# Optimization experiments

Hardware: AMD Instinct MI355X
Metric: run time of the kernel (lower is better)

## Reference

```python
import jax, jax.numpy as jnp
import numpy as np

T, B, D, H = 512, 64, 512, 512


def setup_inputs() -> dict:
    key = jax.random.key(0)
    k_x, k_wi, k_wh = jax.random.split(key, 3)
    x = jax.random.normal(k_x, (T, B, D), dtype=jnp.float32)
    h0 = jnp.zeros((B, H), dtype=jnp.float32)
    # orthogonal(sqrt(2))-like scale approximated with scaled normal weights
    Wi = jax.random.normal(k_wi, (D, 3 * H), dtype=jnp.float32) * (1.0 / np.sqrt(D))
    Wh = jax.random.normal(k_wh, (H, 3 * H), dtype=jnp.float32) * (1.0 / np.sqrt(H))
    bi = jnp.zeros((3 * H,), dtype=jnp.float32)
    bhn = jnp.zeros((H,), dtype=jnp.float32)
    return {"x": x, "h0": h0, "Wi": Wi, "Wh": Wh, "bi": bi, "bhn": bhn}


def reference(x, h0, Wi, Wh, bi, bhn):
    # Flax GRUCell scanned over time. Gate order: (r, z, n).
    # Input path has bias bi; hidden path is bias-free except candidate (bhn).
    def step(h, xt):
        gi = xt @ Wi + bi              # [B, 3H]
        gh = h @ Wh                    # [B, 3H]
        i_r, i_z, i_n = jnp.split(gi, 3, axis=-1)
        h_r, h_z, h_n = jnp.split(gh, 3, axis=-1)
        r = jax.nn.sigmoid(i_r + h_r)
        z = jax.nn.sigmoid(i_z + h_z)
        n = jnp.tanh(i_n + r * (h_n + bhn))
        h_new = (1.0 - z) * n + z * h  # [B, H]
        return h_new, h_new            # y == new hidden state in GRUCell

    _, ys = jax.lax.scan(step, h0, x)  # ys: [T, B, H]; final carry == ys[-1]
    return ys
```

## Files before the change

### kernel.cpp

```cpp
#include <hip/hip_runtime.h>


#define T_STEPS 512
#define NWORK 32
#define CWG 8
#define NCL 4
#define NB_LAUNCH 256
#define FSTRIDE 16

typedef __attribute__((ext_vector_type(8))) short bhalf8;
typedef __attribute__((ext_vector_type(4))) float floatx4;

__device__ inline float bf2f(unsigned short u) {
  union { unsigned u; float f; } v; v.u = ((unsigned)u) << 16; return v.f;
}
__device__ inline unsigned short f2bf(float f) {
  union { float f; unsigned u; } v; v.f = f;
  unsigned x = v.u;
  return (unsigned short)((x + 0x7fffu + ((x >> 16) & 1u)) >> 16);
}

__device__ inline void gload_lds16(const void* g, void* l) {
  __builtin_amdgcn_global_load_lds(
      (const __attribute__((address_space(1))) void*)g,
      (__attribute__((address_space(3))) void*)l, 16, 0, 0);
}

#define O_BAR 0
#define O_HB  4096
#define O_WIT 69632
#define O_WHT 1642496
#define O_GI  3215360
#define O_XB  103878656ULL
#define WS_NEED 137433088ULL

__device__ inline unsigned short* HS(char* ws, int t) {
  return (t == 0) ? (unsigned short*)(ws + O_HB)
                  : (unsigned short*)(ws + O_XB + (long)(t - 1) * 65536);
}

__global__ void prep_kernel(const float* __restrict__ x, const float* __restrict__ h0,
                            const float* __restrict__ Wi, const float* __restrict__ Wh,
                            char* __restrict__ ws) {
  unsigned short* Xb  = (unsigned short*)(ws + O_XB);
  unsigned short* WiT = (unsigned short*)(ws + O_WIT);
  unsigned short* WhT = (unsigned short*)(ws + O_WHT);
  unsigned short* Hb0 = (unsigned short*)(ws + O_HB);
  int* bar = (int*)(ws + O_BAR);
  const long NX = 16777216, NW = 786432, NH = 32768;
  const long total = NX + 2 * NW + NH + 1024;
  for (long i = (long)blockIdx.x * blockDim.x + threadIdx.x; i < total;
       i += (long)gridDim.x * blockDim.x) {
    if (i < NX) {
      Xb[i] = f2bf(x[i]);
    } else if (i < NX + NW) {
      long j = i - NX;
      long n = j >> 9, k = j & 511;
      WiT[j] = f2bf(Wi[k * 1536 + n]);
    } else if (i < NX + 2 * NW) {
      long j = i - NX - NW;
      long n = j >> 9, k = j & 511;
      WhT[j] = f2bf(Wh[k * 1536 + n]);
    } else if (i < NX + 2 * NW + NH) {
      long j = i - NX - 2 * NW;
      Hb0[j] = f2bf(h0[j]);
    } else {
      bar[i - (NX + 2 * NW + NH)] = 0;
    }
  }
}

__global__ void gi_gemm(const unsigned short* __restrict__ Xb,
                        const unsigned short* __restrict__ WiT,
                        const float* __restrict__ bi,
                        unsigned short* __restrict__ Gi) {
  __shared__ unsigned short As[128 * 32];
  __shared__ unsigned short Bs[128 * 32];
  const int tid  = threadIdx.x;
  const int m0   = blockIdx.x * 128;
  const int n0   = blockIdx.y * 128;
  const int lane = tid & 63, wv = tid >> 6;
  const int quad = lane >> 4, l16 = lane & 15;
  const int wm = (wv & 1) * 64, wn = (wv >> 1) * 64;
  const int sr = tid >> 1, sc = (tid & 1) * 16;

  floatx4 acc[4][4] = {};

  for (int kb = 0; kb < 16; ++kb) {
    const int k0 = kb * 32;
    __syncthreads();
    *(bhalf8*)(&As[sr * 32 + sc])     = *(const bhalf8*)(&Xb[(long)(m0 + sr) * 512 + k0 + sc]);
    *(bhalf8*)(&As[sr * 32 + sc + 8]) = *(const bhalf8*)(&Xb[(long)(m0 + sr) * 512 + k0 + sc + 8]);
    *(bhalf8*)(&Bs[sr * 32 + sc])     = *(const bhalf8*)(&WiT[(long)(n0 + sr) * 512 + k0 + sc]);
    *(bhalf8*)(&Bs[sr * 32 + sc + 8]) = *(const bhalf8*)(&WiT[(long)(n0 + sr) * 512 + k0 + sc + 8]);
    __syncthreads();

    bhalf8 af[4], bf[4];
#pragma unroll
    for (int i = 0; i < 4; ++i)
      af[i] = *(const bhalf8*)(&As[(wm + i * 16 + l16) * 32 + quad * 8]);
#pragma unroll
    for (int j = 0; j < 4; ++j)
      bf[j] = *(const bhalf8*)(&Bs[(wn + j * 16 + l16) * 32 + quad * 8]);
#pragma unroll
    for (int i = 0; i < 4; ++i)
#pragma unroll
      for (int j = 0; j < 4; ++j)
        acc[i][j] = __builtin_amdgcn_mfma_f32_16x16x32_bf16(af[i], bf[j], acc[i][j], 0, 0, 0);
  }

#pragma unroll
  for (int i = 0; i < 4; ++i)
#pragma unroll
    for (int j = 0; j < 4; ++j) {
      const int col = n0 + wn + j * 16 + l16;
      const float bv = bi[col];
#pragma unroll
      for (int r = 0; r < 4; ++r) {
        const int row = m0 + wm + i * 16 + quad * 4 + r;
        Gi[(long)row * 1536 + col] = f2bf(acc[i][j][r] + bv);
      }
    }
}

__launch_bounds__(256, 1)
__global__ void recurrent_kernel(char* __restrict__ ws,
                                 const float* __restrict__ h0,
                                 const float* __restrict__ bhn,
                                 float* __restrict__ out) {
  const unsigned short* WhT = (const unsigned short*)(ws + O_WHT);
  const unsigned short* Gi  = (const unsigned short*)(ws + O_GI);
  int* bar     = (int*)(ws + O_BAR);
  int* fflag   = bar;
  int* flags   = bar + 512;
  int* tick    = bar + 544;
  int* arrived = bar + 552;
  int* tick2   = bar + 553;
  int* abortf  = bar + 555;
  int* arrive2 = bar + 556;

  const int tid = threadIdx.x;
  __shared__ __align__(64) unsigned char smem[16384];
  __shared__ int sdec[4];

  if (tid == 0) {
    const int xcc = (int)(__builtin_amdgcn_s_getreg((3 << 11) | 20)) & 7;
    const int slot = __hip_atomic_fetch_add(&tick[xcc], 1, __ATOMIC_SEQ_CST, __HIP_MEMORY_SCOPE_AGENT);
    __hip_atomic_fetch_add(arrived, 1, __ATOMIC_SEQ_CST, __HIP_MEMORY_SCOPE_AGENT);
    while (__hip_atomic_load(arrived, __ATOMIC_ACQUIRE, __HIP_MEMORY_SCOPE_AGENT) < NB_LAUNCH)
      __builtin_amdgcn_s_sleep(4);
    int cnts[8];
    for (int c = 0; c < 8; ++c)
      cnts[c] = __hip_atomic_load(&tick[c], __ATOMIC_ACQUIRE, __HIP_MEMORY_SCOPE_AGENT);
    int chosen[NCL]; bool used[8] = {false,false,false,false,false,false,false,false};
    for (int k = 0; k < NCL; ++k) {
      int best = -1, bi2 = 0;
      for (int c = 0; c < 8; ++c)
        if (!used[c] && cnts[c] > best) { best = cnts[c]; bi2 = c; }
      chosen[k] = bi2; used[bi2] = true;
    }
    const int fastc = (cnts[chosen[NCL - 1]] >= CWG) ? 1 : 0;
    int cl = -1, sl = -1;
    if (fastc) {
      for (int k = 0; k < NCL; ++k)
        if (xcc == chosen[k] && slot < CWG) { cl = k; sl = slot; }
    } else {
      const int s2 = __hip_atomic_fetch_add(tick2, 1, __ATOMIC_SEQ_CST, __HIP_MEMORY_SCOPE_AGENT);
      if (s2 < NWORK) { cl = s2 >> 3; sl = s2 & 7; }
    }
    sdec[0] = fastc; sdec[1] = cl; sdec[2] = sl;
  }
  __syncthreads();
  const int fastc   = sdec[0];
  const int cluster = sdec[1];
  const int slot    = sdec[2];
  if (cluster < 0) return;

  if (tid == 0) {
    int mode = 0;
    if (fastc) {
      int* pc = bar + 576 + cluster * 16;
      __hip_atomic_fetch_add(pc, 1, __ATOMIC_RELAXED, __HIP_MEMORY_SCOPE_WORKGROUP);
      int ok = 0;
      for (int it = 0; it < 200000; ++it) {
        int exp = CWG;
        if (__hip_atomic_compare_exchange_strong(pc, &exp, CWG,
                __ATOMIC_RELAXED, __ATOMIC_RELAXED, __HIP_MEMORY_SCOPE_WORKGROUP)) { ok = 1; break; }
      }
      if (!ok) __hip_atomic_fetch_add(abortf, 1, __ATOMIC_RELAXED, __HIP_MEMORY_SCOPE_AGENT);
      __hip_atomic_fetch_add(arrive2, 1, __ATOMIC_ACQ_REL, __HIP_MEMORY_SCOPE_AGENT);
      while (__hip_atomic_load(arrive2, __ATOMIC_ACQUIRE, __HIP_MEMORY_SCOPE_AGENT) < NWORK)
        __builtin_amdgcn_s_sleep(2);
      mode = (__hip_atomic_load(abortf, __ATOMIC_ACQUIRE, __HIP_MEMORY_SCOPE_AGENT) > 0) ? 0 : 1;
    }
    sdec[3] = mode;
  }
  __syncthreads();
  const int fast = sdec[3];

  const int wv   = tid >> 6;
  const int lane = tid & 63;
  const int quad = lane >> 4, l16 = lane & 15;
  const int gcol = slot * 64 + wv * 16 + l16;
  const int brow0 = cluster * 16 + quad * 4;

  bhalf8 Bf[3][16];
#pragma unroll
  for (int gt = 0; gt < 3; ++gt) {
    const unsigned short* wp = WhT + (long)(gt * 512 + gcol) * 512;
#pragma unroll
    for (int ks = 0; ks < 16; ++ks)
      Bf[gt][ks] = *(const bhalf8*)(wp + ks * 32 + quad * 8);
  }
  const float bhn_v = bhn[gcol];

  float hprev[4];
#pragma unroll
  for (int r = 0; r < 4; ++r)
    hprev[r] = h0[(brow0 + r) * 512 + gcol];

  float gi_r[4], gi_z[4], gi_n[4];
#pragma unroll
  for (int r = 0; r < 4; ++r) {
    const long gb = (long)(brow0 + r) * 1536 + gcol;
    gi_r[r] = bf2f(Gi[gb]);
    gi_z[r] = bf2f(Gi[gb + 512]);
    gi_n[r] = bf2f(Gi[gb + 1024]);
  }

  for (int t = 0; t < T_STEPS; ++t) {
    const unsigned short* hin  = HS(ws, t);
    unsigned short*       hout = HS(ws, t + 1);

    bhalf8 af[16];
    if (fast) {
      const char* hbase = (const char*)hin + (size_t)cluster * 16384;
#pragma unroll
      for (int it = 0; it < 4; ++it) {
        const int row = wv * 4 + it;
        const char* src = hbase + row * 1024 + ((lane * 16) ^ ((row & 7) << 4));
        gload_lds16(src, &smem[row * 1024]);
      }
      __syncthreads();
    }

    float nr[4], nz[4], nn[4];
    if (t + 1 < T_STEPS) {
      const long gibase = (long)(t + 1) * 64 * 1536;
#pragma unroll
      for (int r = 0; r < 4; ++r) {
        const long gb = gibase + (long)(brow0 + r) * 1536 + gcol;
        nr[r] = bf2f(Gi[gb]);
        nz[r] = bf2f(Gi[gb + 512]);
        nn[r] = bf2f(Gi[gb + 1024]);
      }
    }

    if (fast) {
#pragma unroll
      for (int ks = 0; ks < 16; ++ks) {
        const int byteoff = (l16 << 10) + (((ks << 6) + (quad << 4)) ^ ((l16 & 7) << 4));
        af[ks] = *(const bhalf8*)(&smem[byteoff]);
      }
    } else {
      const unsigned short* ap = hin + (cluster * 16 + l16) * 512 + quad * 8;
#pragma unroll
      for (int ks = 0; ks < 16; ++ks) {
        union { unsigned long long q[2]; bhalf8 v; } u;
        u.q[0] = __hip_atomic_load((const unsigned long long*)(ap + ks * 32),
                                   __ATOMIC_RELAXED, __HIP_MEMORY_SCOPE_AGENT);
        u.q[1] = __hip_atomic_load((const unsigned long long*)(ap + ks * 32) + 1,
                                   __ATOMIC_RELAXED, __HIP_MEMORY_SCOPE_AGENT);
        af[ks] = u.v;
      }
    }

    floatx4 racc = {0.f, 0.f, 0.f, 0.f};
    floatx4 zacc = {0.f, 0.f, 0.f, 0.f};
    floatx4 nacc = {0.f, 0.f, 0.f, 0.f};
#pragma unroll
    for (int ks = 0; ks < 16; ++ks) {
      racc = __builtin_amdgcn_mfma_f32_16x16x32_bf16(af[ks], Bf[0][ks], racc, 0, 0, 0);
      zacc = __builtin_amdgcn_mfma_f32_16x16x32_bf16(af[ks], Bf[1][ks], zacc, 0, 0, 0);
      nacc = __builtin_amdgcn_mfma_f32_16x16x32_bf16(af[ks], Bf[2][ks], nacc, 0, 0, 0);
    }

#pragma unroll
    for (int r = 0; r < 4; ++r) {
      const int brow = brow0 + r;
      const float rg = 1.f / (1.f + __expf(-(gi_r[r] + racc[r])));
      const float zg = 1.f / (1.f + __expf(-(gi_z[r] + zacc[r])));
      const float pre = gi_n[r] + rg * (nacc[r] + bhn_v);
      const float e2 = __expf(2.f * pre);
      const float ng = 1.f - 2.f / (e2 + 1.f);
      const float hn = (1.f - zg) * ng + zg * hprev[r];
      hprev[r] = hn;
      const unsigned hb = (unsigned)f2bf(hn);
      const unsigned ob = __shfl_xor(hb, 1, 64);
      if (!(l16 & 1)) {
        unsigned* dst = (unsigned*)(hout + brow * 512 + gcol);
        const unsigned packed = hb | (ob << 16);
        if (fast) *dst = packed;
        else __hip_atomic_store(dst, packed, __ATOMIC_RELAXED, __HIP_MEMORY_SCOPE_AGENT);
      }
    }

    if (t + 1 < T_STEPS) {
#pragma unroll
      for (int r = 0; r < 4; ++r) { gi_r[r] = nr[r]; gi_z[r] = nz[r]; gi_n[r] = nn[r]; }

      const int want = t + 1;
      if (fast) {
        __syncthreads();
        if (tid == 0)
          __hip_atomic_store(&fflag[(cluster * CWG + slot) * FSTRIDE], want,
                             __ATOMIC_RELAXED, __HIP_MEMORY_SCOPE_WORKGROUP);
#pragma unroll
        for (int r = 0; r < 4; ++r)
          out[((long)t * 64 + brow0 + r) * 512 + gcol] = hprev[r];
        if (tid < 64) {
          bool ok = (lane >= CWG);
          while (!__all(ok)) {
            if (!ok) {
              int exp = want;
              __hip_atomic_compare_exchange_strong(&fflag[(cluster * CWG + lane) * FSTRIDE],
                  &exp, want, __ATOMIC_RELAXED, __ATOMIC_RELAXED, __HIP_MEMORY_SCOPE_WORKGROUP);
              ok = (exp >= want);
            }
          }
        }
        __syncthreads();
      } else {
#pragma unroll
        for (int r = 0; r < 4; ++r)
          out[((long)t * 64 + brow0 + r) * 512 + gcol] = hprev[r];
        __syncthreads();
        if (tid == 0)
          __hip_atomic_store(&flags[cluster * CWG + slot], want,
                             __ATOMIC_RELAXED, __HIP_MEMORY_SCOPE_AGENT);
        int v;
        do {
          v = __hip_atomic_load(&flags[cluster * CWG + (lane & 7)],
                                __ATOMIC_RELAXED, __HIP_MEMORY_SCOPE_AGENT);
        } while (!__all(v >= want));
        __atomic_signal_fence(__ATOMIC_SEQ_CST);
      }
    } else {
#pragma unroll
      for (int r = 0; r < 4; ++r)
        out[((long)t * 64 + brow0 + r) * 512 + gcol] = hprev[r];
    }
  }
}

extern "C" void kernel_launch(void* const* d_in, const int* in_sizes, int n_in,
                              void* d_out, int out_size, void* d_ws, size_t ws_size,
                              hipStream_t stream) {
  const float* x   = (const float*)d_in[0];
  const float* h0  = (const float*)d_in[1];
  const float* Wi  = (const float*)d_in[2];
  const float* Wh  = (const float*)d_in[3];
  const float* bi  = (const float*)d_in[4];
  const float* bhn = (const float*)d_in[5];
  float* out = (float*)d_out;
  char* ws = (char*)d_ws;
  if (ws_size < WS_NEED) return;

  prep_kernel<<<4096, 256, 0, stream>>>(x, h0, Wi, Wh, ws);
  gi_gemm<<<dim3(256, 12), 256, 0, stream>>>(
      (const unsigned short*)(ws + O_XB), (const unsigned short*)(ws + O_WIT),
      bi, (unsigned short*)(ws + O_GI));
  recurrent_kernel<<<NB_LAUNCH, 256, 0, stream>>>(ws, h0, bhn, out);
}
```

Measured before the change: 1.723 ms.

## Load hidden state directly from global and ping-pong Gi prefetch buffers

Removes the LDS staging path (global_load_lds into swizzled shared memory plus a __syncthreads) for the fast path, reading the h fragments directly from global into registers. The Gi prefetch for the next step moves after the flag publish, overlapping the barrier wait, and is held as raw bf16 in two ping-pong register arrays with the time loop manually unrolled by two to avoid copies. This aims to shorten the per-step critical path but relies on plain loads seeing other workgroups' freshly written h through the cache, and redundantly loads h per wave instead of sharing via LDS.

```diff
diff --git a/kernel.cpp b/kernel.cpp
--- a/kernel.cpp
+++ b/kernel.cpp
@@ -18,12 +18,6 @@
   union { float f; unsigned u; } v; v.f = f;
   unsigned x = v.u;
   return (unsigned short)((x + 0x7fffu + ((x >> 16) & 1u)) >> 16);
-}
-
-__device__ inline void gload_lds16(const void* g, void* l) {
-  __builtin_amdgcn_global_load_lds(
-      (const __attribute__((address_space(1))) void*)g,
-      (__attribute__((address_space(3))) void*)l, 16, 0, 0);
 }
 
 #define O_BAR 0
@@ -123,6 +117,122 @@
     }
 }
 
+#define GRU_STEP(T_, CUR_, NXT_) do {                                              \
+    const int t_ = (T_);                                                           \
+    const unsigned short* hin  = HS(ws, t_);                                       \
+    unsigned short*       hout = HS(ws, t_ + 1);                                   \
+    const unsigned short* ap = hin + (cluster * 16 + l16) * 512 + quad * 8;        \
+    bhalf8 af[16];                                                                 \
+    if (fast) {                                                                    \
+      _Pragma("unroll")                                                            \
+      for (int ks = 0; ks < 16; ++ks)                                              \
+        af[ks] = *(const bhalf8*)(ap + ks * 32);          \
+    } else {                                                                       \
+      _Pragma("unroll")                                                            \
+      for (int ks = 0; ks < 16; ++ks) {                                            \
+        union { unsigned long long q[2]; bhalf8 v; } u;                            \
+        u.q[0] = __hip_atomic_load((const unsigned long long*)(ap + ks * 32),      \
+                                   __ATOMIC_RELAXED, __HIP_MEMORY_SCOPE_AGENT);    \
+        u.q[1] = __hip_atomic_load((const unsigned long long*)(ap + ks * 32) + 1,  \
+                                   __ATOMIC_RELAXED, __HIP_MEMORY_SCOPE_AGENT);    \
+        af[ks] = u.v;                                                              \
+      }                                                                            \
+    }                                                                              \
+    floatx4 racc = {0.f, 0.f, 0.f, 0.f};                                           \
+    floatx4 zacc = {0.f, 0.f, 0.f, 0.f};                                           \
+    floatx4 nacc = {0.f, 0.f, 0.f, 0.f};                                           \
+    _Pragma("unroll")                                                              \
+    for (int ks = 0; ks < 16; ++ks) {                                              \
+      racc = __builtin_amdgcn_mfma_f32_16x16x32_bf16(af[ks], Bf[0][ks], racc, 0, 0, 0);\
+      zacc = __builtin_amdgcn_mfma_f32_16x16x32_bf16(af[ks], Bf[1][ks], zacc, 0, 0, 0);\
+      nacc = __builtin_amdgcn_mfma_f32_16x16x32_bf16(af[ks], Bf[2][ks], nacc, 0, 0, 0);\
+    }                                                                              \
+    _Pragma("unroll")                                                              \
+    for (int r = 0; r < 4; ++r) {                                                  \
+      const float rg = 1.f / (1.f + __expf(-(bf2f(CUR_[r]) + racc[r])));           \
+      const float zg = 1.f / (1.f + __expf(-(bf2f(CUR_[4 + r]) + zacc[r])));       \
+      const float pre = bf2f(CUR_[8 + r]) + rg * (nacc[r] + bhn_v);                \
+      const float e2 = __expf(2.f * pre);                                          \
+      const float ng = 1.f - 2.f / (e2 + 1.f);                           \
+      const float hn = (1.f - zg) * ng + zg * hprev[r];                            \
+      hprev[r] = hn;                                                               \
+      const unsigned hb = (unsigned)f2bf(hn);                                      \
+      const unsigned ob = __shfl_xor(hb, 1, 64);          \
+      if (!(l16 & 1)) {                                                            \
+        unsigned* dst = (unsigned*)(hout + (brow0 + r) * 512 + gcol);              \
+        const unsigned packed = hb | (ob << 16);                                   \
+        if (fast) *dst = packed;                      \
+        else __hip_atomic_store(dst, packed, __ATOMIC_RELAXED,                     \
+                                __HIP_MEMORY_SCOPE_AGENT);                         \
+      }                                                                            \
+    }                                                                              \
+    if (t_ + 1 < T_STEPS) {                                                        \
+      const int want = t_ + 1;                                                     \
+      if (fast) {                                                                  \
+        __syncthreads();                         \
+        if (tid == 0)                                                              \
+          __hip_atomic_store(&fflag[(cluster * CWG + slot) * FSTRIDE], want,       \
+                             __ATOMIC_RELAXED, __HIP_MEMORY_SCOPE_WORKGROUP);      \
+         \
+        _Pragma("unroll")                                                          \
+        for (int r = 0; r < 4; ++r)                                                \
+          out[((long)t_ * 64 + brow0 + r) * 512 + gcol] = hprev[r];                \
+        {                                                                          \
+          const long gibase = (long)want * 64 * 1536;                              \
+          _Pragma("unroll")                                                        \
+          for (int r = 0; r < 4; ++r) {                                            \
+            const long gb = gibase + (long)(brow0 + r) * 1536 + gcol;              \
+            NXT_[r]     = Gi[gb];               \
+            NXT_[4 + r] = Gi[gb + 512];          \
+            NXT_[8 + r] = Gi[gb + 1024];                                           \
+          }                                                                        \
+        }                                                                          \
+        if (tid < 64) {                                                            \
+          bool ok = (lane >= CWG);                                                 \
+          while (!__all(ok)) {                                                     \
+            if (!ok) {                                                             \
+              int exp = want;                                                      \
+              __hip_atomic_compare_exchange_strong(                                \
+                  &fflag[(cluster * CWG + lane) * FSTRIDE], &exp, want,            \
+                  __ATOMIC_RELAXED, __ATOMIC_RELAXED,                              \
+                  __HIP_MEMORY_SCOPE_WORKGROUP);                                   \
+              ok = (exp >= want);                                                  \
+            }                                                                      \
+          }                                                                        \
+        }                                                                          \
+        __syncthreads();                                   \
+      } else {                                                                     \
+        _Pragma("unroll")                                                          \
+        for (int r = 0; r < 4; ++r)                                                \
+          out[((long)t_ * 64 + brow0 + r) * 512 + gcol] = hprev[r];                \
+        {                                                                          \
+          const long gibase = (long)want * 64 * 1536;                              \
+          _Pragma("unroll")                                                        \
+          for (int r = 0; r < 4; ++r) {                                            \
+            const long gb = gibase + (long)(brow0 + r) * 1536 + gcol;              \
+            NXT_[r]     = Gi[gb];                                                  \
+            NXT_[4 + r] = Gi[gb + 512];                                            \
+            NXT_[8 + r] = Gi[gb + 1024];                                           \
+          }                                                                        \
+        }                                                                          \
+        __syncthreads();                                                           \
+        if (tid == 0)                                                              \
+          __hip_atomic_store(&flags[cluster * CWG + slot], want,                   \
+                             __ATOMIC_RELAXED, __HIP_MEMORY_SCOPE_AGENT);          \
+        int v;                                                                     \
+        do {                                                                       \
+          v = __hip_atomic_load(&flags[cluster * CWG + (lane & 7)],                \
+                                __ATOMIC_RELAXED, __HIP_MEMORY_SCOPE_AGENT);       \
+        } while (!__all(v >= want));                                               \
+        __atomic_signal_fence(__ATOMIC_SEQ_CST);                                   \
+      }                                                                            \
+    } else {                                                                       \
+      _Pragma("unroll")                                                            \
+      for (int r = 0; r < 4; ++r)                                                  \
+        out[((long)t_ * 64 + brow0 + r) * 512 + gcol] = hprev[r];                  \
+    }                                                                              \
+  } while (0)
+
 __launch_bounds__(256, 1)
 __global__ void recurrent_kernel(char* __restrict__ ws,
                                  const float* __restrict__ h0,
@@ -140,7 +250,6 @@
   int* arrive2 = bar + 556;
 
   const int tid = threadIdx.x;
-  __shared__ __align__(64) unsigned char smem[16384];
   __shared__ int sdec[4];
 
   if (tid == 0) {
@@ -219,137 +328,19 @@
   for (int r = 0; r < 4; ++r)
     hprev[r] = h0[(brow0 + r) * 512 + gcol];
 
-  float gi_r[4], gi_z[4], gi_n[4];
+  unsigned short giA[12], giB[12];
 #pragma unroll
   for (int r = 0; r < 4; ++r) {
     const long gb = (long)(brow0 + r) * 1536 + gcol;
-    gi_r[r] = bf2f(Gi[gb]);
-    gi_z[r] = bf2f(Gi[gb + 512]);
-    gi_n[r] = bf2f(Gi[gb + 1024]);
-  }
-
-  for (int t = 0; t < T_STEPS; ++t) {
-    const unsigned short* hin  = HS(ws, t);
-    unsigned short*       hout = HS(ws, t + 1);
-
-    bhalf8 af[16];
-    if (fast) {
-      const char* hbase = (const char*)hin + (size_t)cluster * 16384;
-#pragma unroll
-      for (int it = 0; it < 4; ++it) {
-        const int row = wv * 4 + it;
-        const char* src = hbase + row * 1024 + ((lane * 16) ^ ((row & 7) << 4));
-        gload_lds16(src, &smem[row * 1024]);
-      }
-      __syncthreads();
-    }
-
-    float nr[4], nz[4], nn[4];
-    if (t + 1 < T_STEPS) {
-      const long gibase = (long)(t + 1) * 64 * 1536;
-#pragma unroll
-      for (int r = 0; r < 4; ++r) {
-        const long gb = gibase + (long)(brow0 + r) * 1536 + gcol;
-        nr[r] = bf2f(Gi[gb]);
-        nz[r] = bf2f(Gi[gb + 512]);
-        nn[r] = bf2f(Gi[gb + 1024]);
-      }
-    }
-
-    if (fast) {
-#pragma unroll
-      for (int ks = 0; ks < 16; ++ks) {
-        const int byteoff = (l16 << 10) + (((ks << 6) + (quad << 4)) ^ ((l16 & 7) << 4));
-        af[ks] = *(const bhalf8*)(&smem[byteoff]);
-      }
-    } else {
-      const unsigned short* ap = hin + (cluster * 16 + l16) * 512 + quad * 8;
-#pragma unroll
-      for (int ks = 0; ks < 16; ++ks) {
-        union { unsigned long long q[2]; bhalf8 v; } u;
-        u.q[0] = __hip_atomic_load((const unsigned long long*)(ap + ks * 32),
-                                   __ATOMIC_RELAXED, __HIP_MEMORY_SCOPE_AGENT);
-        u.q[1] = __hip_atomic_load((const unsigned long long*)(ap + ks * 32) + 1,
-                                   __ATOMIC_RELAXED, __HIP_MEMORY_SCOPE_AGENT);
-        af[ks] = u.v;
-      }
-    }
-
-    floatx4 racc = {0.f, 0.f, 0.f, 0.f};
-    floatx4 zacc = {0.f, 0.f, 0.f, 0.f};
-    floatx4 nacc = {0.f, 0.f, 0.f, 0.f};
-#pragma unroll
-    for (int ks = 0; ks < 16; ++ks) {
-      racc = __builtin_amdgcn_mfma_f32_16x16x32_bf16(af[ks], Bf[0][ks], racc, 0, 0, 0);
-      zacc = __builtin_amdgcn_mfma_f32_16x16x32_bf16(af[ks], Bf[1][ks], zacc, 0, 0, 0);
-      nacc = __builtin_amdgcn_mfma_f32_16x16x32_bf16(af[ks], Bf[2][ks], nacc, 0, 0, 0);
-    }
-
-#pragma unroll
-    for (int r = 0; r < 4; ++r) {
-      const int brow = brow0 + r;
-      const float rg = 1.f / (1.f + __expf(-(gi_r[r] + racc[r])));
-      const float zg = 1.f / (1.f + __expf(-(gi_z[r] + zacc[r])));
-      const float pre = gi_n[r] + rg * (nacc[r] + bhn_v);
-      const float e2 = __expf(2.f * pre);
-      const float ng = 1.f - 2.f / (e2 + 1.f);
-      const float hn = (1.f - zg) * ng + zg * hprev[r];
-      hprev[r] = hn;
-      const unsigned hb = (unsigned)f2bf(hn);
-      const unsigned ob = __shfl_xor(hb, 1, 64);
-      if (!(l16 & 1)) {
-        unsigned* dst = (unsigned*)(hout + brow * 512 + gcol);
-        const unsigned packed = hb | (ob << 16);
-        if (fast) *dst = packed;
-        else __hip_atomic_store(dst, packed, __ATOMIC_RELAXED, __HIP_MEMORY_SCOPE_AGENT);
-      }
-    }
-
-    if (t + 1 < T_STEPS) {
-#pragma unroll
-      for (int r = 0; r < 4; ++r) { gi_r[r] = nr[r]; gi_z[r] = nz[r]; gi_n[r] = nn[r]; }
-
-      const int want = t + 1;
-      if (fast) {
-        __syncthreads();
-        if (tid == 0)
-          __hip_atomic_store(&fflag[(cluster * CWG + slot) * FSTRIDE], want,
-                             __ATOMIC_RELAXED, __HIP_MEMORY_SCOPE_WORKGROUP);
-#pragma unroll
-        for (int r = 0; r < 4; ++r)
-          out[((long)t * 64 + brow0 + r) * 512 + gcol] = hprev[r];
-        if (tid < 64) {
-          bool ok = (lane >= CWG);
-          while (!__all(ok)) {
-            if (!ok) {
-              int exp = want;
-              __hip_atomic_compare_exchange_strong(&fflag[(cluster * CWG + lane) * FSTRIDE],
-                  &exp, want, __ATOMIC_RELAXED, __ATOMIC_RELAXED, __HIP_MEMORY_SCOPE_WORKGROUP);
-              ok = (exp >= want);
-            }
-          }
-        }
-        __syncthreads();
-      } else {
-#pragma unroll
-        for (int r = 0; r < 4; ++r)
-          out[((long)t * 64 + brow0 + r) * 512 + gcol] = hprev[r];
-        __syncthreads();
-        if (tid == 0)
-          __hip_atomic_store(&flags[cluster * CWG + slot], want,
-                             __ATOMIC_RELAXED, __HIP_MEMORY_SCOPE_AGENT);
-        int v;
-        do {
-          v = __hip_atomic_load(&flags[cluster * CWG + (lane & 7)],
-                                __ATOMIC_RELAXED, __HIP_MEMORY_SCOPE_AGENT);
-        } while (!__all(v >= want));
-        __atomic_signal_fence(__ATOMIC_SEQ_CST);
-      }
-    } else {
-#pragma unroll
-      for (int r = 0; r < 4; ++r)
-        out[((long)t * 64 + brow0 + r) * 512 + gcol] = hprev[r];
-    }
+    giA[r]     = Gi[gb];
+    giA[4 + r] = Gi[gb + 512];
+    giA[8 + r] = Gi[gb + 1024];
+  }
+
+#pragma unroll 1
+  for (int tt = 0; tt < T_STEPS; tt += 2) {
+    GRU_STEP(tt,     giA, giB);
+    GRU_STEP(tt + 1, giB, giA);
   }
 }
 
```

New measurement: 2.035 ms. 18.1% more time.
